# Optimization experiments

Measured on AMD Instinct MI355X. Metric: run time of the kernel, lower is better.

The kernel has to match this reference:

```python
import jax, jax.numpy as jnp
import numpy as np
from jax import lax

# ---- constants matching init_kwargs ----
NY, NX = 1024, 1024
DX, DY = 50.0, 50.0
TTOT = 32.0
DTMAX = 0.5
RHO, G, FD = 910.0, 9.81, 1e-17
EPS = 1e-10
T_FREQ = 5.0
N_STEPS = 64            # fixed step count (>= TTOT/DTMAX); dt masked to 0 once time >= TTOT
LAPSE = 0.0065          # degC per m elevation lapse rate (SMB model)
MELT_FACTOR = 0.5       # m ice / (degC * yr) ablation factor (SMB model)


def update_smb(Z_surf, precip, T_ma_lowest, T_mj_lowest, ice_mask):
    # Lapse-rate temperatures at the surface
    T_ma = T_ma_lowest - LAPSE * Z_surf   # mean annual temperature
    T_mj = T_mj_lowest - LAPSE * Z_surf   # mean July temperature
    accumulation = precip * (T_ma < 0.0).astype(Z_surf.dtype)
    ablation = MELT_FACTOR * jnp.maximum(T_mj, 0.0)
    return (accumulation - ablation) * ice_mask


def setup_inputs() -> dict:
    key = jax.random.key(0)
    k1, k2, k3 = jax.random.split(key, 3)
    # smooth mountain topography: 2500 m gaussian massif + small noise
    y = np.arange(NY, dtype=np.float32) * DY
    x = np.arange(NX, dtype=np.float32) * DX
    yy, xx = np.meshgrid(y, x, indexing="ij")
    cy, cx = y.mean(), x.mean()
    sigma = 0.25 * NX * DX
    z = 2500.0 * np.exp(-((yy - cy) ** 2 + (xx - cx) ** 2) / (2.0 * sigma ** 2))
    Z_topo = jnp.asarray(z, dtype=jnp.float32) + 5.0 * jax.random.normal(k1, (NY, NX), dtype=jnp.float32)
    precip_tensor = 2.0 * jax.random.uniform(k2, (NY, NX), dtype=jnp.float32)  # m ice / yr
    T_ma_lowest = jnp.float32(8.0) + jax.random.normal(k3, (), dtype=jnp.float32)
    T_mj_lowest = T_ma_lowest + jnp.float32(8.0)
    ice_mask = jnp.ones((NY, NX), dtype=jnp.float32)
    return {"precip_tensor": precip_tensor, "T_ma_lowest": T_ma_lowest,
            "T_mj_lowest": T_mj_lowest, "Z_topo": Z_topo, "ice_mask": ice_mask}


def _glacier_step(carry, _, Z_topo, precip, T_ma_lowest, T_mj_lowest, ice_mask):
    H_ice, Z_surf, smb, time, t_last = carry
    # staggered-grid averages and slopes (SIA diffusion)
    H_avg = 0.25 * (H_ice[:-1, :-1] + H_ice[1:, 1:] + H_ice[:-1, 1:] + H_ice[1:, :-1])
    Sx = (Z_surf[:, 1:] - Z_surf[:, :-1]) / DX
    Sy = (Z_surf[1:, :] - Z_surf[:-1, :]) / DY
    Sx = 0.5 * (Sx[:-1, :] + Sx[1:, :])          # (NY-1, NX-1)
    Sy = 0.5 * (Sy[:, :-1] + Sy[:, 1:])          # (NY-1, NX-1)
    Snorm = jnp.sqrt(Sx ** 2 + Sy ** 2 + EPS)
    D = FD * (RHO * G) ** 3 * H_avg ** 5 * Snorm ** 2 + EPS
    # adaptive CFL dt; torch uses .item() so dt is a non-differentiable constant
    dt = jnp.minimum(min(DX, DY) ** 2 / (2.7 * jnp.max(D)), DTMAX)
    dt = lax.stop_gradient(dt)
    dt = jnp.where(time < TTOT, dt, 0.0)         # freeze once ttot is reached
    qx = -(0.5 * (D[:-1, :] + D[1:, :])) * (Z_surf[1:-1, 1:] - Z_surf[1:-1, :-1]) / DX
    qy = -(0.5 * (D[:, :-1] + D[:, 1:])) * (Z_surf[1:, 1:-1] - Z_surf[:-1, 1:-1]) / DY
    dHdt = -(jnp.diff(qx, axis=1) / DX + jnp.diff(qy, axis=0) / DY)  # (NY-2, NX-2)
    H_new = H_ice.at[1:-1, 1:-1].add(dt * (dHdt + smb[1:-1, 1:-1]))
    H_new = jnp.maximum(H_new, 0.0)
    Z_new = Z_topo + H_new
    time = time + dt
    # refresh SMB every T_FREQ model years
    do_upd = (time - t_last) >= T_FREQ
    smb_new = update_smb(Z_new, precip, T_ma_lowest, T_mj_lowest, ice_mask)
    smb = jnp.where(do_upd, smb_new, smb)
    t_last = jnp.where(do_upd, time, t_last)
    return (H_new, Z_new, smb, time, t_last), None


def reference(precip_tensor, T_ma_lowest, T_mj_lowest, Z_topo, ice_mask):
    H_ice = jnp.zeros((NY, NX), dtype=jnp.float32)
    Z_surf = Z_topo + H_ice
    smb = update_smb(Z_surf, precip_tensor, T_ma_lowest, T_mj_lowest, ice_mask)
    time = jnp.float32(0.0)
    t_last = jnp.float32(0.0)
    step = lambda c, x: _glacier_step(c, x, Z_topo, precip_tensor, T_ma_lowest, T_mj_lowest, ice_mask)
    (H_ice, _, _, _, _), _ = lax.scan(step, (H_ice, Z_surf, smb, time, t_last), None, length=N_STEPS)
    return H_ice
```

## Files before the change

### kernel.cpp

```cpp
#include <hip/hip_runtime.h>
#include <math.h>

#define NYg 1024
#define NXg 1024
#define W   1024
#define NSTEPS 64
#define NBLK 256
#define EN (NBLK * W)

#define WS_SLOTS 0
#define NSLOTW   ((NSTEPS + 1) * NBLK)
#define WS_NBF   24576
#define WS_CTRL_END 32768
#define WS_GRIDS 32768

constexpr float DXf   = 50.0f;
constexpr float DYf   = 50.0f;
constexpr float TTOTf = 32.0f;
constexpr float DTMAXf= 0.5f;
constexpr float EPSf  = 1e-10f;
constexpr float TFREQ = 5.0f;
constexpr float LAPSE = 0.0065f;
constexpr float MELTF = 0.5f;
constexpr double RHOG = 910.0 * 9.81;
constexpr float  CDf  = (float)(1e-17 * RHOG * RHOG * RHOG);

__device__ __forceinline__ float scloadf(const float* p) {
    return __hip_atomic_load(p, __ATOMIC_RELAXED, __HIP_MEMORY_SCOPE_SYSTEM);
}
__device__ __forceinline__ void scstoref(float* p, float v) {
    __hip_atomic_store(p, v, __ATOMIC_RELAXED, __HIP_MEMORY_SCOPE_SYSTEM);
}
__device__ __forceinline__ unsigned scloadu(const unsigned* p) {
    return __hip_atomic_load(p, __ATOMIC_RELAXED, __HIP_MEMORY_SCOPE_SYSTEM);
}

__device__ __forceinline__ float dfunc(float h00, float h01, float h10, float h11,
                                       float z00, float z01, float z10, float z11)
{
    float havg = 0.25f * (h00 + h11 + h01 + h10);
    float sx = ((z01 - z00) + (z11 - z10)) * (0.5f / DXf);
    float sy = ((z10 - z00) + (z11 - z01)) * (0.5f / DYf);
    float sn = sqrtf(sx * sx + sy * sy + EPSf);
    float h2 = havg * havg;
    float h4 = h2 * h2;
    return CDf * (h4 * havg) * (sn * sn) + EPSf;
}

__global__ __launch_bounds__(256) void k_init(unsigned* __restrict__ ctrl)
{
    int idx = blockIdx.x * blockDim.x + threadIdx.x;
    int stride = gridDim.x * blockDim.x;
    for (int i = idx; i < WS_CTRL_END; i += stride) {
        unsigned v = 0u;
        if (i < NBLK) v = __float_as_uint(EPSf);
        ctrl[i] = v;
    }
}

__global__ __launch_bounds__(1024, 1) void k_run(
    float* __restrict__ EZa0, float* __restrict__ EZa1,
    float* __restrict__ EZb0, float* __restrict__ EZb1,
    float* __restrict__ EDa0, float* __restrict__ EDa1,
    float* __restrict__ EDb0, float* __restrict__ EDb1,
    const float* __restrict__ ztopo, const float* __restrict__ precip,
    const float* __restrict__ mask, const float* __restrict__ tma,
    const float* __restrict__ tmj, unsigned* __restrict__ ctrl,
    float* __restrict__ Hout)
{
    __shared__ float sZ[5][W];
    __shared__ float sH[5][W];
    __shared__ float sD[4][W];
    __shared__ float smax16[16];
    __shared__ float smax4[4];

    float*    slotsf = (float*)ctrl + WS_SLOTS;
    unsigned* nbf    = ctrl + WS_NBF;

    const int c   = threadIdx.x;
    const int b   = blockIdx.x;
    const int r0  = b * 4;
    const int lane = c & 63, wid = c >> 6;
    const bool hasA = (b > 0), hasB = (b < NBLK - 1);
    const bool cL = (c >= 1), cR = (c <= NXg - 2);
    const int cm = (c == 0) ? 0 : c - 1;
    const int cp = (c == W - 1) ? W - 1 : c + 1;

    const float TMA = tma[0], TMJ = tmj[0];

    float z_[7];
    float h_[5];
    float dreg[4];
    float dtop, dtopL;
    float dbot, dbotL;
    float smbr[5], ztr[5];

    #pragma unroll
    for (int q = 0; q < 7; ++q) {
        int r = r0 - 1 + q;
        z_[q] = (r >= 0 && r < NYg) ? ztopo[r * W + c] : 0.0f;
    }
    #pragma unroll
    for (int rr = 0; rr < 5; ++rr) {
        int r = r0 + rr;
        h_[rr] = 0.0f;
        if (r < NYg) {
            float z = z_[rr + 1];
            ztr[rr] = z;
            float t_ma = TMA - LAPSE * z;
            float t_mj = TMJ - LAPSE * z;
            float acc  = (t_ma < 0.0f) ? precip[r * W + c] : 0.0f;
            float abl  = MELTF * fmaxf(t_mj, 0.0f);
            smbr[rr] = (acc - abl) * mask[r * W + c];
            sZ[rr][c] = z;
            sH[rr][c] = 0.0f;
        } else {
            ztr[rr] = 0.0f; smbr[rr] = 0.0f;
            sZ[rr][c] = 0.0f;
            sH[rr][c] = 0.0f;
        }
    }
    dtop = EPSf; dtopL = EPSf; dbot = EPSf; dbotL = EPSf;
    #pragma unroll
    for (int q = 0; q < 4; ++q) { dreg[q] = EPSf; sD[q][c] = EPSf; }
    __syncthreads();

    float t = 0.0f, tl = 0.0f;

    for (int s = 0; s < NSTEPS; ++s) {
        const float* EZar = (s & 1) ? EZa1 : EZa0;
        float*       EZaw = (s & 1) ? EZa0 : EZa1;
        const float* EZbr = (s & 1) ? EZb1 : EZb0;
        float*       EZbw = (s & 1) ? EZb0 : EZb1;
        const float* EDar = (s & 1) ? EDa1 : EDa0;
        float*       EDaw = (s & 1) ? EDa0 : EDa1;
        const float* EDbr = (s & 1) ? EDb1 : EDb0;
        float*       EDbw = (s & 1) ? EDb0 : EDb1;

        if (s > 0) {
            if (hasA)
                while (scloadu(&nbf[(b - 1) * 32]) < (unsigned)s) __builtin_amdgcn_s_sleep(1);
            if (hasB)
                while (scloadu(&nbf[(b + 1) * 32]) < (unsigned)s) __builtin_amdgcn_s_sleep(1);
            if (hasA) {
                z_[0] = scloadf(EZbr + (b - 1) * W + c);
                if (cR) dtop  = scloadf(EDbr + (b - 1) * W + c);
                if (cL) dtopL = scloadf(EDbr + (b - 1) * W + (c-1));
            }
            if (hasB) {
                z_[6] = scloadf(EZar + (b + 1) * W + c);
                if (cR) dbot  = scloadf(EDar + (b + 1) * W + c);
                if (cL) dbotL = scloadf(EDar + (b + 1) * W + (c-1));
            }
        }

        float dl[6], doa[6];
        dl[0] = dtopL;      doa[0] = dtop;
        dl[1] = sD[0][cm];  doa[1] = dreg[0];
        dl[2] = sD[1][cm];  doa[2] = dreg[1];
        dl[3] = sD[2][cm];  doa[3] = dreg[2];
        dl[4] = sD[3][cm];  doa[4] = dreg[3];
        dl[5] = dbotL;      doa[5] = dbot;

        float zl[5], zr[5];
        #pragma unroll
        for (int q = 0; q < 5; ++q) { zl[q] = sZ[q][cm]; zr[q] = sZ[q][cp]; }

        float qy[6];
        #pragma unroll
        for (int k = 0; k < 6; ++k)
            qy[k] = -0.5f * (dl[k] + doa[k]) * (z_[k + 1] - z_[k]) * (1.0f / DYf);

        float dh[5];
        bool  inter[5];
        #pragma unroll
        for (int rr = 0; rr < 5; ++rr) {
            int r = r0 + rr;
            bool iv = (r >= 1 && r <= NYg - 2 && cL && cR);
            float zc  = z_[rr + 1];
            float qxR = -0.5f * (doa[rr] + doa[rr + 1]) * (zr[rr] - zc) * (1.0f / DXf);
            float qxL = -0.5f * (dl[rr]  + dl[rr + 1])  * (zc - zl[rr]) * (1.0f / DXf);
            float d = -((qxR - qxL) * (1.0f / DXf) + (qy[rr + 1] - qy[rr]) * (1.0f / DYf));
            dh[rr] = iv ? d : 0.0f;
            inter[rr] = iv;
        }

        if (c < NBLK) {
            const float* sl = slotsf + s * NBLK + c;
            float v = scloadf(sl);
            while (__float_as_uint(v) == 0u) { __builtin_amdgcn_s_sleep(1); v = scloadf(sl); }
            #pragma unroll
            for (int off = 32; off >= 1; off >>= 1)
                v = fmaxf(v, __shfl_xor(v, off, 64));
            if (lane == 0) smax4[wid] = v;
        }
        __syncthreads();

        float mD = fmaxf(fmaxf(smax4[0], smax4[1]), fmaxf(smax4[2], smax4[3]));
        float dt = fminf(2500.0f / (2.7f * mD), DTMAXf);
        if (!(t < TTOTf)) dt = 0.0f;
        float nt  = t + dt;
        bool  upd = (nt - tl) >= TFREQ;

        #pragma unroll
        for (int rr = 0; rr < 5; ++rr) {
            int r = r0 + rr;
            if (r < NYg) {
                float h, z;
                if (inter[rr]) { h = fmaxf(h_[rr] + dt * (dh[rr] + smbr[rr]), 0.0f);
                                 z = ztr[rr] + h; }
                else           { h = 0.0f; z = z_[rr + 1]; }
                h_[rr] = h; z_[rr + 1] = z;
                sZ[rr][c] = z;
                sH[rr][c] = h;
                if (rr == 1 && hasA) scstoref(EZaw + b * W + c, z);
                if (rr == 3 && hasB) scstoref(EZbw + b * W + c, z);
                if (upd) {
                    float t_ma = TMA - LAPSE * z;
                    float t_mj = TMJ - LAPSE * z;
                    float acc  = (t_ma < 0.0f) ? precip[r * W + c] : 0.0f;
                    float abl  = MELTF * fmaxf(t_mj, 0.0f);
                    smbr[rr] = (acc - abl) * mask[r * W + c];
                }
            } else {
                h_[rr] = 0.0f;
            }
        }
        __syncthreads();

        if (s < NSTEPS - 1) {
            float m = 0.0f;
            float dv[4];
            #pragma unroll
            for (int rr = 0; rr < 4; ++rr) {
                int i = r0 + rr;
                float dd = 0.0f;
                if (i <= NYg - 2 && cR) {
                    dd = dfunc(h_[rr], sH[rr][c + 1],
                               h_[rr + 1], sH[rr + 1][c + 1],
                               z_[rr + 1], sZ[rr][c + 1],
                               z_[rr + 2], sZ[rr + 1][c + 1]);
                    m = fmaxf(m, dd);
                    if (rr == 0 && hasA) scstoref(EDaw + b * W + c, dd);
                    if (rr == 3 && hasB) scstoref(EDbw + b * W + c, dd);
                }
                dv[rr] = dd;
            }
            sD[0][c] = dv[0];
            sD[1][c] = dv[1];
            sD[2][c] = dv[2];
            sD[3][c] = dv[3];
            dreg[0] = dv[0]; dreg[1] = dv[1]; dreg[2] = dv[2]; dreg[3] = dv[3];
            #pragma unroll
            for (int off = 32; off >= 1; off >>= 1)
                m = fmaxf(m, __shfl_xor(m, off, 64));
            if (lane == 0) smax16[wid] = m;
            __syncthreads();
            if (c == 0) {
                #pragma unroll
                for (int q = 1; q < 16; ++q) m = fmaxf(m, smax16[q]);
                scstoref(slotsf + (s + 1) * NBLK + b, m);
            }
            asm volatile("s_waitcnt vmcnt(0)" ::: "memory");
            __syncthreads();
            if (c == 0)
                __hip_atomic_store(&nbf[b * 32], (unsigned)(s + 1),
                                   __ATOMIC_RELAXED, __HIP_MEMORY_SCOPE_SYSTEM);
        }

        t = nt;
        if (upd) tl = nt;
    }

    #pragma unroll
    for (int rr = 0; rr < 4; ++rr)
        Hout[(r0 + rr) * W + c] = h_[rr];
}

extern "C" void kernel_launch(void* const* d_in, const int* in_sizes, int n_in,
                              void* d_out, int out_size, void* d_ws, size_t ws_size,
                              hipStream_t stream)
{
    const float* precip = (const float*)d_in[0];
    const float* tma    = (const float*)d_in[1];
    const float* tmj    = (const float*)d_in[2];
    const float* ztopo  = (const float*)d_in[3];
    const float* mask   = (const float*)d_in[4];

    unsigned* ctrl = (unsigned*)d_ws;
    float* g = (float*)d_ws + WS_GRIDS;
    float* EZa0 = g + 0 * EN; float* EZa1 = g + 1 * EN;
    float* EZb0 = g + 2 * EN; float* EZb1 = g + 3 * EN;
    float* EDa0 = g + 4 * EN; float* EDa1 = g + 5 * EN;
    float* EDb0 = g + 6 * EN; float* EDb1 = g + 7 * EN;

    k_init<<<dim3(64), dim3(256), 0, stream>>>(ctrl);

    k_run<<<dim3(256), dim3(1024), 0, stream>>>(EZa0, EZa1, EZb0, EZb1,
                                                EDa0, EDa1, EDb0, EDb1,
                                                ztopo, precip, mask, tma, tmj,
                                                ctrl, (float*)d_out);
}
```

Baseline: 393.5 us.

## Replace per-block ready flags with step-tagged 64-bit halo values

```diff
diff --git a/kernel.cpp b/kernel.cpp
--- a/kernel.cpp
+++ b/kernel.cpp
@@ -8,11 +8,10 @@
 #define NBLK 256
 #define EN (NBLK * W)
 
-#define WS_SLOTS 0
-#define NSLOTW   ((NSTEPS + 1) * NBLK)
-#define WS_NBF   24576
-#define WS_CTRL_END 32768
-#define WS_GRIDS 32768
+typedef unsigned long long ull;
+
+#define WS_CTRL_DW 32768
+#define WS_TOTAL_U4 ((WS_CTRL_DW * 4 + 8 * EN * 8) / 16)
 
 constexpr float DXf   = 50.0f;
 constexpr float DYf   = 50.0f;
@@ -31,8 +30,14 @@
 __device__ __forceinline__ void scstoref(float* p, float v) {
     __hip_atomic_store(p, v, __ATOMIC_RELAXED, __HIP_MEMORY_SCOPE_SYSTEM);
 }
-__device__ __forceinline__ unsigned scloadu(const unsigned* p) {
+__device__ __forceinline__ ull scload64(const ull* p) {
     return __hip_atomic_load(p, __ATOMIC_RELAXED, __HIP_MEMORY_SCOPE_SYSTEM);
+}
+__device__ __forceinline__ void scstore64(ull* p, ull v) {
+    __hip_atomic_store(p, v, __ATOMIC_RELAXED, __HIP_MEMORY_SCOPE_SYSTEM);
+}
+__device__ __forceinline__ ull packtv(unsigned tag, float v) {
+    return ((ull)tag << 32) | (ull)__float_as_uint(v);
 }
 
 __device__ __forceinline__ float dfunc(float h00, float h01, float h10, float h11,
@@ -47,22 +52,23 @@
     return CDf * (h4 * havg) * (sn * sn) + EPSf;
 }
 
-__global__ __launch_bounds__(256) void k_init(unsigned* __restrict__ ctrl)
+__global__ __launch_bounds__(256) void k_init(uint4* __restrict__ ws)
 {
     int idx = blockIdx.x * blockDim.x + threadIdx.x;
     int stride = gridDim.x * blockDim.x;
-    for (int i = idx; i < WS_CTRL_END; i += stride) {
-        unsigned v = 0u;
-        if (i < NBLK) v = __float_as_uint(EPSf);
-        ctrl[i] = v;
+    const unsigned e = __float_as_uint(EPSf);
+    for (int i = idx; i < (int)WS_TOTAL_U4; i += stride) {
+        uint4 v = make_uint4(0u, 0u, 0u, 0u);
+        if (i < NBLK / 4) v = make_uint4(e, e, e, e);
+        ws[i] = v;
     }
 }
 
 __global__ __launch_bounds__(1024, 1) void k_run(
-    float* __restrict__ EZa0, float* __restrict__ EZa1,
-    float* __restrict__ EZb0, float* __restrict__ EZb1,
-    float* __restrict__ EDa0, float* __restrict__ EDa1,
-    float* __restrict__ EDb0, float* __restrict__ EDb1,
+    ull* __restrict__ EZa0, ull* __restrict__ EZa1,
+    ull* __restrict__ EZb0, ull* __restrict__ EZb1,
+    ull* __restrict__ EDa0, ull* __restrict__ EDa1,
+    ull* __restrict__ EDb0, ull* __restrict__ EDb1,
     const float* __restrict__ ztopo, const float* __restrict__ precip,
     const float* __restrict__ mask, const float* __restrict__ tma,
     const float* __restrict__ tmj, unsigned* __restrict__ ctrl,
@@ -74,8 +80,7 @@
     __shared__ float smax16[16];
     __shared__ float smax4[4];
 
-    float*    slotsf = (float*)ctrl + WS_SLOTS;
-    unsigned* nbf    = ctrl + WS_NBF;
+    float* slotsf = (float*)ctrl;
 
     const int c   = threadIdx.x;
     const int b   = blockIdx.x;
@@ -128,30 +133,48 @@
     float t = 0.0f, tl = 0.0f;
 
     for (int s = 0; s < NSTEPS; ++s) {
-        const float* EZar = (s & 1) ? EZa1 : EZa0;
-        float*       EZaw = (s & 1) ? EZa0 : EZa1;
-        const float* EZbr = (s & 1) ? EZb1 : EZb0;
-        float*       EZbw = (s & 1) ? EZb0 : EZb1;
-        const float* EDar = (s & 1) ? EDa1 : EDa0;
-        float*       EDaw = (s & 1) ? EDa0 : EDa1;
-        const float* EDbr = (s & 1) ? EDb1 : EDb0;
-        float*       EDbw = (s & 1) ? EDb0 : EDb1;
+        const ull* EZar = (s & 1) ? EZa1 : EZa0;
+        ull*       EZaw = (s & 1) ? EZa0 : EZa1;
+        const ull* EZbr = (s & 1) ? EZb1 : EZb0;
+        ull*       EZbw = (s & 1) ? EZb0 : EZb1;
+        const ull* EDar = (s & 1) ? EDa1 : EDa0;
+        ull*       EDaw = (s & 1) ? EDa0 : EDa1;
+        const ull* EDbr = (s & 1) ? EDb1 : EDb0;
+        ull*       EDbw = (s & 1) ? EDb0 : EDb1;
 
         if (s > 0) {
-            if (hasA)
-                while (scloadu(&nbf[(b - 1) * 32]) < (unsigned)s) __builtin_amdgcn_s_sleep(1);
-            if (hasB)
-                while (scloadu(&nbf[(b + 1) * 32]) < (unsigned)s) __builtin_amdgcn_s_sleep(1);
-            if (hasA) {
-                z_[0] = scloadf(EZbr + (b - 1) * W + c);
-                if (cR) dtop  = scloadf(EDbr + (b - 1) * W + c);
-                if (cL) dtopL = scloadf(EDbr + (b - 1) * W + (c-1));
+            const unsigned tg = (unsigned)s;
+            const ull RD = ((ull)tg << 32);
+            ull vzt = RD, vdt = RD, vdtl = RD, vzb = RD, vdb = RD, vdbl = RD;
+            const ull* pZt  = EZbr + (b - 1) * W + c;
+            const ull* pDt  = EDbr + (b - 1) * W + c;
+            const ull* pDtl = EDbr + (b - 1) * W + (c - 1);
+            const ull* pZb  = EZar + (b + 1) * W + c;
+            const ull* pDb  = EDar + (b + 1) * W + c;
+            const ull* pDbl = EDar + (b + 1) * W + (c - 1);
+            for (;;) {
+                if (hasA) {
+                    vzt = scload64(pZt);
+                    if (cR) vdt  = scload64(pDt);
+                    if (cL) vdtl = scload64(pDtl);
+                }
+                if (hasB) {
+                    vzb = scload64(pZb);
+                    if (cR) vdb  = scload64(pDb);
+                    if (cL) vdbl = scload64(pDbl);
+                }
+                bool ok = ((unsigned)(vzt  >> 32) == tg) & ((unsigned)(vdt  >> 32) == tg)
+                        & ((unsigned)(vdtl >> 32) == tg) & ((unsigned)(vzb  >> 32) == tg)
+                        & ((unsigned)(vdb  >> 32) == tg) & ((unsigned)(vdbl >> 32) == tg);
+                if (ok) break;
+                __builtin_amdgcn_s_sleep(1);
             }
-            if (hasB) {
-                z_[6] = scloadf(EZar + (b + 1) * W + c);
-                if (cR) dbot  = scloadf(EDar + (b + 1) * W + c);
-                if (cL) dbotL = scloadf(EDar + (b + 1) * W + (c-1));
-            }
+            if (hasA) z_[0] = __uint_as_float((unsigned)vzt);
+            if (hasB) z_[6] = __uint_as_float((unsigned)vzb);
+            if (hasA && cR) dtop  = __uint_as_float((unsigned)vdt);
+            if (hasA && cL) dtopL = __uint_as_float((unsigned)vdtl);
+            if (hasB && cR) dbot  = __uint_as_float((unsigned)vdb);
+            if (hasB && cL) dbotL = __uint_as_float((unsigned)vdbl);
         }
 
         float dl[6], doa[6];
@@ -213,8 +236,8 @@
                 h_[rr] = h; z_[rr + 1] = z;
                 sZ[rr][c] = z;
                 sH[rr][c] = h;
-                if (rr == 1 && hasA) scstoref(EZaw + b * W + c, z);
-                if (rr == 3 && hasB) scstoref(EZbw + b * W + c, z);
+                if (rr == 1 && hasA) scstore64(EZaw + b * W + c, packtv((unsigned)(s + 1), z));
+                if (rr == 3 && hasB) scstore64(EZbw + b * W + c, packtv((unsigned)(s + 1), z));
                 if (upd) {
                     float t_ma = TMA - LAPSE * z;
                     float t_mj = TMJ - LAPSE * z;
@@ -241,8 +264,8 @@
                                z_[rr + 1], sZ[rr][c + 1],
                                z_[rr + 2], sZ[rr + 1][c + 1]);
                     m = fmaxf(m, dd);
-                    if (rr == 0 && hasA) scstoref(EDaw + b * W + c, dd);
-                    if (rr == 3 && hasB) scstoref(EDbw + b * W + c, dd);
+                    if (rr == 0 && hasA) scstore64(EDaw + b * W + c, packtv((unsigned)(s + 1), dd));
+                    if (rr == 3 && hasB) scstore64(EDbw + b * W + c, packtv((unsigned)(s + 1), dd));
                 }
                 dv[rr] = dd;
             }
@@ -261,11 +284,6 @@
                 for (int q = 1; q < 16; ++q) m = fmaxf(m, smax16[q]);
                 scstoref(slotsf + (s + 1) * NBLK + b, m);
             }
-            asm volatile("s_waitcnt vmcnt(0)" ::: "memory");
-            __syncthreads();
-            if (c == 0)
-                __hip_atomic_store(&nbf[b * 32], (unsigned)(s + 1),
-                                   __ATOMIC_RELAXED, __HIP_MEMORY_SCOPE_SYSTEM);
         }
 
         t = nt;
@@ -288,13 +306,13 @@
     const float* mask   = (const float*)d_in[4];
 
     unsigned* ctrl = (unsigned*)d_ws;
-    float* g = (float*)d_ws + WS_GRIDS;
-    float* EZa0 = g + 0 * EN; float* EZa1 = g + 1 * EN;
-    float* EZb0 = g + 2 * EN; float* EZb1 = g + 3 * EN;
-    float* EDa0 = g + 4 * EN; float* EDa1 = g + 5 * EN;
-    float* EDb0 = g + 6 * EN; float* EDb1 = g + 7 * EN;
-
-    k_init<<<dim3(64), dim3(256), 0, stream>>>(ctrl);
+    ull* hp = (ull*)((char*)d_ws + WS_CTRL_DW * 4);
+    ull* EZa0 = hp + 0 * EN; ull* EZa1 = hp + 1 * EN;
+    ull* EZb0 = hp + 2 * EN; ull* EZb1 = hp + 3 * EN;
+    ull* EDa0 = hp + 4 * EN; ull* EDa1 = hp + 5 * EN;
+    ull* EDb0 = hp + 6 * EN; ull* EDb1 = hp + 7 * EN;
+
+    k_init<<<dim3(2048), dim3(256), 0, stream>>>((uint4*)d_ws);
 
     k_run<<<dim3(256), dim3(1024), 0, stream>>>(EZa0, EZa1, EZb0, EZb1,
                                                 EDa0, EDa1, EDb0, EDb1,
```

New measurement: 443.4 us. +12.7%, slower.

## Replace per-block slot grid barrier with packed 64-bit counter and thresholded max

Applied to the files above, without the earlier changes.

```diff
diff --git a/kernel.cpp b/kernel.cpp
--- a/kernel.cpp
+++ b/kernel.cpp
@@ -8,8 +8,8 @@
 #define NBLK 256
 #define EN (NBLK * W)
 
-#define WS_SLOTS 0
-#define NSLOTW   ((NSTEPS + 1) * NBLK)
+typedef unsigned long long ull;
+
 #define WS_NBF   24576
 #define WS_CTRL_END 32768
 #define WS_GRIDS 32768
@@ -22,6 +22,7 @@
 constexpr float TFREQ = 5.0f;
 constexpr float LAPSE = 0.0065f;
 constexpr float MELTF = 0.5f;
+constexpr float THf   = 1800.0f;
 constexpr double RHOG = 910.0 * 9.81;
 constexpr float  CDf  = (float)(1e-17 * RHOG * RHOG * RHOG);
 
@@ -32,6 +33,9 @@
     __hip_atomic_store(p, v, __ATOMIC_RELAXED, __HIP_MEMORY_SCOPE_SYSTEM);
 }
 __device__ __forceinline__ unsigned scloadu(const unsigned* p) {
+    return __hip_atomic_load(p, __ATOMIC_RELAXED, __HIP_MEMORY_SCOPE_SYSTEM);
+}
+__device__ __forceinline__ ull scload64(const ull* p) {
     return __hip_atomic_load(p, __ATOMIC_RELAXED, __HIP_MEMORY_SCOPE_SYSTEM);
 }
 
@@ -53,7 +57,7 @@
     int stride = gridDim.x * blockDim.x;
     for (int i = idx; i < WS_CTRL_END; i += stride) {
         unsigned v = 0u;
-        if (i < NBLK) v = __float_as_uint(EPSf);
+        if (i == 0) v = (unsigned)NBLK;
         ctrl[i] = v;
     }
 }
@@ -72,10 +76,9 @@
     __shared__ float sH[5][W];
     __shared__ float sD[4][W];
     __shared__ float smax16[16];
-    __shared__ float smax4[4];
-
-    float*    slotsf = (float*)ctrl + WS_SLOTS;
-    unsigned* nbf    = ctrl + WS_NBF;
+
+    ull*      cntAlarm = (ull*)ctrl;
+    unsigned* nbf      = ctrl + WS_NBF;
 
     const int c   = threadIdx.x;
     const int b   = blockIdx.x;
@@ -93,7 +96,7 @@
     float dreg[4];
     float dtop, dtopL;
     float dbot, dbotL;
-    float smbr[5], ztr[5];
+    float smbr[5], ztr[5], pr_[5], mk_[5];
 
     #pragma unroll
     for (int q = 0; q < 7; ++q) {
@@ -107,15 +110,17 @@
         if (r < NYg) {
             float z = z_[rr + 1];
             ztr[rr] = z;
+            pr_[rr] = precip[r * W + c];
+            mk_[rr] = mask[r * W + c];
             float t_ma = TMA - LAPSE * z;
             float t_mj = TMJ - LAPSE * z;
-            float acc  = (t_ma < 0.0f) ? precip[r * W + c] : 0.0f;
+            float acc  = (t_ma < 0.0f) ? pr_[rr] : 0.0f;
             float abl  = MELTF * fmaxf(t_mj, 0.0f);
-            smbr[rr] = (acc - abl) * mask[r * W + c];
+            smbr[rr] = (acc - abl) * mk_[rr];
             sZ[rr][c] = z;
             sH[rr][c] = 0.0f;
         } else {
-            ztr[rr] = 0.0f; smbr[rr] = 0.0f;
+            ztr[rr] = 0.0f; smbr[rr] = 0.0f; pr_[rr] = 0.0f; mk_[rr] = 0.0f;
             sZ[rr][c] = 0.0f;
             sH[rr][c] = 0.0f;
         }
@@ -185,18 +190,15 @@
             inter[rr] = iv;
         }
 
-        if (c < NBLK) {
-            const float* sl = slotsf + s * NBLK + c;
-            float v = scloadf(sl);
-            while (__float_as_uint(v) == 0u) { __builtin_amdgcn_s_sleep(1); v = scloadf(sl); }
-            #pragma unroll
-            for (int off = 32; off >= 1; off >>= 1)
-                v = fmaxf(v, __shfl_xor(v, off, 64));
-            if (lane == 0) smax4[wid] = v;
-        }
+        const ull* ca = cntAlarm + s;
+        ull v = scload64(ca);
+        while ((unsigned)v != (unsigned)NBLK) {
+            __builtin_amdgcn_s_sleep(1);
+            v = scload64(ca);
+        }
+        float mD = fmaxf(__uint_as_float((unsigned)(v >> 32)), EPSf);
         __syncthreads();
 
-        float mD = fmaxf(fmaxf(smax4[0], smax4[1]), fmaxf(smax4[2], smax4[3]));
         float dt = fminf(2500.0f / (2.7f * mD), DTMAXf);
         if (!(t < TTOTf)) dt = 0.0f;
         float nt  = t + dt;
@@ -218,9 +220,9 @@
                 if (upd) {
                     float t_ma = TMA - LAPSE * z;
                     float t_mj = TMJ - LAPSE * z;
-                    float acc  = (t_ma < 0.0f) ? precip[r * W + c] : 0.0f;
+                    float acc  = (t_ma < 0.0f) ? pr_[rr] : 0.0f;
                     float abl  = MELTF * fmaxf(t_mj, 0.0f);
-                    smbr[rr] = (acc - abl) * mask[r * W + c];
+                    smbr[rr] = (acc - abl) * mk_[rr];
                 }
             } else {
                 h_[rr] = 0.0f;
@@ -259,7 +261,14 @@
             if (c == 0) {
                 #pragma unroll
                 for (int q = 1; q < 16; ++q) m = fmaxf(m, smax16[q]);
-                scstoref(slotsf + (s + 1) * NBLK + b, m);
+                unsigned* cw = (unsigned*)(cntAlarm + (s + 1));
+                if (m > THf) {
+                    __hip_atomic_fetch_max(cw + 1, __float_as_uint(m),
+                                           __ATOMIC_RELAXED, __HIP_MEMORY_SCOPE_SYSTEM);
+                    asm volatile("s_waitcnt vmcnt(0)" ::: "memory");
+                }
+                __hip_atomic_fetch_add(cw, 1u,
+                                       __ATOMIC_RELAXED, __HIP_MEMORY_SCOPE_SYSTEM);
             }
             asm volatile("s_waitcnt vmcnt(0)" ::: "memory");
             __syncthreads();
```

Measured after the change: 523.6 us. 1.33x slower.

## Publish halo diffusivity rows early before interior rows and max reduction

Applied to the files above, without the earlier changes.

```diff
diff --git a/kernel.cpp b/kernel.cpp
--- a/kernel.cpp
+++ b/kernel.cpp
@@ -9,7 +9,6 @@
 #define EN (NBLK * W)
 
 #define WS_SLOTS 0
-#define NSLOTW   ((NSTEPS + 1) * NBLK)
 #define WS_NBF   24576
 #define WS_CTRL_END 32768
 #define WS_GRIDS 32768
@@ -74,7 +73,7 @@
     __shared__ float smax16[16];
     __shared__ float smax4[4];
 
-    float*    slotsf = (float*)ctrl + WS_SLOTS;
+    float*    slotsf = (float*)ctrl;
     unsigned* nbf    = ctrl + WS_NBF;
 
     const int c   = threadIdx.x;
@@ -93,7 +92,7 @@
     float dreg[4];
     float dtop, dtopL;
     float dbot, dbotL;
-    float smbr[5], ztr[5];
+    float smbr[5], ztr[5], pr_[5], mk_[5];
 
     #pragma unroll
     for (int q = 0; q < 7; ++q) {
@@ -107,15 +106,17 @@
         if (r < NYg) {
             float z = z_[rr + 1];
             ztr[rr] = z;
+            pr_[rr] = precip[r * W + c];
+            mk_[rr] = mask[r * W + c];
             float t_ma = TMA - LAPSE * z;
             float t_mj = TMJ - LAPSE * z;
-            float acc  = (t_ma < 0.0f) ? precip[r * W + c] : 0.0f;
+            float acc  = (t_ma < 0.0f) ? pr_[rr] : 0.0f;
             float abl  = MELTF * fmaxf(t_mj, 0.0f);
-            smbr[rr] = (acc - abl) * mask[r * W + c];
+            smbr[rr] = (acc - abl) * mk_[rr];
             sZ[rr][c] = z;
             sH[rr][c] = 0.0f;
         } else {
-            ztr[rr] = 0.0f; smbr[rr] = 0.0f;
+            ztr[rr] = 0.0f; smbr[rr] = 0.0f; pr_[rr] = 0.0f; mk_[rr] = 0.0f;
             sZ[rr][c] = 0.0f;
             sH[rr][c] = 0.0f;
         }
@@ -218,9 +219,9 @@
                 if (upd) {
                     float t_ma = TMA - LAPSE * z;
                     float t_mj = TMJ - LAPSE * z;
-                    float acc  = (t_ma < 0.0f) ? precip[r * W + c] : 0.0f;
+                    float acc  = (t_ma < 0.0f) ? pr_[rr] : 0.0f;
                     float abl  = MELTF * fmaxf(t_mj, 0.0f);
-                    smbr[rr] = (acc - abl) * mask[r * W + c];
+                    smbr[rr] = (acc - abl) * mk_[rr];
                 }
             } else {
                 h_[rr] = 0.0f;
@@ -229,28 +230,34 @@
         __syncthreads();
 
         if (s < NSTEPS - 1) {
-            float m = 0.0f;
-            float dv[4];
-            #pragma unroll
-            for (int rr = 0; rr < 4; ++rr) {
-                int i = r0 + rr;
-                float dd = 0.0f;
-                if (i <= NYg - 2 && cR) {
-                    dd = dfunc(h_[rr], sH[rr][c + 1],
-                               h_[rr + 1], sH[rr + 1][c + 1],
-                               z_[rr + 1], sZ[rr][c + 1],
-                               z_[rr + 2], sZ[rr + 1][c + 1]);
-                    m = fmaxf(m, dd);
-                    if (rr == 0 && hasA) scstoref(EDaw + b * W + c, dd);
-                    if (rr == 3 && hasB) scstoref(EDbw + b * W + c, dd);
-                }
-                dv[rr] = dd;
-            }
-            sD[0][c] = dv[0];
-            sD[1][c] = dv[1];
-            sD[2][c] = dv[2];
-            sD[3][c] = dv[3];
-            dreg[0] = dv[0]; dreg[1] = dv[1]; dreg[2] = dv[2]; dreg[3] = dv[3];
+            float dv0 = 0.0f, dv1 = 0.0f, dv2 = 0.0f, dv3 = 0.0f;
+            if (r0 + 0 <= NYg - 2 && cR) {
+                dv0 = dfunc(h_[0], sH[0][c + 1], h_[1], sH[1][c + 1],
+                            z_[1], sZ[0][c + 1], z_[2], sZ[1][c + 1]);
+                if (hasA) scstoref(EDaw + b * W + c, dv0);
+            }
+            if (r0 + 3 <= NYg - 2 && cR) {
+                dv3 = dfunc(h_[3], sH[3][c + 1], h_[4], sH[4][c + 1],
+                            z_[4], sZ[3][c + 1], z_[5], sZ[4][c + 1]);
+                if (hasB) scstoref(EDbw + b * W + c, dv3);
+            }
+            sD[0][c] = dv0;
+            sD[3][c] = dv3;
+            asm volatile("s_waitcnt vmcnt(0)" ::: "memory");
+            __syncthreads();
+            if (c == 0)
+                __hip_atomic_store(&nbf[b * 32], (unsigned)(s + 1),
+                                   __ATOMIC_RELAXED, __HIP_MEMORY_SCOPE_SYSTEM);
+            if (r0 + 1 <= NYg - 2 && cR)
+                dv1 = dfunc(h_[1], sH[1][c + 1], h_[2], sH[2][c + 1],
+                            z_[2], sZ[1][c + 1], z_[3], sZ[2][c + 1]);
+            if (r0 + 2 <= NYg - 2 && cR)
+                dv2 = dfunc(h_[2], sH[2][c + 1], h_[3], sH[3][c + 1],
+                            z_[3], sZ[2][c + 1], z_[4], sZ[3][c + 1]);
+            sD[1][c] = dv1;
+            sD[2][c] = dv2;
+            dreg[0] = dv0; dreg[1] = dv1; dreg[2] = dv2; dreg[3] = dv3;
+            float m = fmaxf(fmaxf(dv0, dv1), fmaxf(dv2, dv3));
             #pragma unroll
             for (int off = 32; off >= 1; off >>= 1)
                 m = fmaxf(m, __shfl_xor(m, off, 64));
@@ -261,11 +268,6 @@
                 for (int q = 1; q < 16; ++q) m = fmaxf(m, smax16[q]);
                 scstoref(slotsf + (s + 1) * NBLK + b, m);
             }
-            asm volatile("s_waitcnt vmcnt(0)" ::: "memory");
-            __syncthreads();
-            if (c == 0)
-                __hip_atomic_store(&nbf[b * 32], (unsigned)(s + 1),
-                                   __ATOMIC_RELAXED, __HIP_MEMORY_SCOPE_SYSTEM);
         }
 
         t = nt;
```

Measured after the change: 433.0 us. 10.0% more time.
